# Performance work log

Measured on AMD Instinct MI355X. Metric: run time of the kernel, lower is better.

Reference implementation:

```python
import jax, jax.numpy as jnp
import numpy as np

EPS = 1e-8  # matches torch cosine_similarity default eps


def setup_inputs() -> dict:
    key = jax.random.key(0)
    k1, k2 = jax.random.split(key)
    B, S, D = 64, 512, 768
    logits = jax.random.normal(k1, (B, S, D), dtype=jnp.float32)
    labels = jax.random.randint(k2, (B, S), 0, 10, dtype=jnp.int64)
    return {"logits": logits, "labels": labels, "entity_id": 5}


def reference(logits, labels, entity_id):
    # --- get_proto: mean of token vectors whose label == entity_id,
    # excluding sequence position 0 (label_idx.remove(0) in the original) ---
    B, S, D = logits.shape
    pos = jnp.arange(S)
    ent_mask = (labels == entity_id) & (pos[None, :] != 0)      # [B,S]
    m = ent_mask.astype(logits.dtype)
    num_ent = jnp.maximum(m.sum(), 1.0)
    proto = jnp.einsum('bs,bsd->d', m, logits) / num_ent        # [D]

    # --- CLLoss: mean cosine similarity between proto and every token
    # with a nonzero label ---
    nz_mask = (labels != 0).astype(logits.dtype)                # [B,S]
    dots = jnp.einsum('bsd,d->bs', logits, proto)               # [B,S]
    denom = jnp.linalg.norm(logits, axis=-1) * jnp.linalg.norm(proto)
    sims = dots / jnp.maximum(denom, EPS)                       # [B,S]
    num_tok = jnp.maximum(nz_mask.sum(), 1.0)
    loss = (sims * nz_mask).sum() / num_tok
    return loss
```

## Files before the change

kernel.cpp:

```cpp
#include <hip/hip_runtime.h>
#include <math.h>

#define DD 768
#define S_LEN 512
#define NF4 3
#define NACC (2 * DD + 1)
#define PW 1544
#define GMAIN 1024
#define NYB 16
#define BCHUNK (GMAIN / NYB)

__global__ __launch_bounds__(256) void main_pass(const float* __restrict__ logits,
                                                 const int* __restrict__ labels,
                                                 const int* __restrict__ eid_p,
                                                 int ntok,
                                                 float* __restrict__ partial) {
    const int eid  = *eid_p;
    const int lane = threadIdx.x & 63;
    const int wid  = threadIdx.x >> 6;
    const int gw   = blockIdx.x * 4 + wid;
    const int nw   = GMAIN * 4;

    float u_acc[12], p_acc[12];
#pragma unroll
    for (int j = 0; j < 12; ++j) { u_acc[j] = 0.f; p_acc[j] = 0.f; }
    float tokcnt = 0.f;

    for (int t = gw; t < ntok; t += 2 * nw) {
        const int t2 = t + nw;
        const bool has2 = (t2 < ntok);

        const float4* src0 = (const float4*)(logits + (size_t)t * DD);
        const float4* src1 = (const float4*)(logits + (size_t)(has2 ? t2 : t) * DD);
        float4 f0[NF4], f1[NF4];
#pragma unroll
        for (int k = 0; k < NF4; ++k) f0[k] = src0[k * 64 + lane];
#pragma unroll
        for (int k = 0; k < NF4; ++k) f1[k] = src1[k * 64 + lane];

        float ss0 = 0.f, ss1 = 0.f;
#pragma unroll
        for (int k = 0; k < NF4; ++k) {
            ss0 += f0[k].x * f0[k].x + f0[k].y * f0[k].y + f0[k].z * f0[k].z + f0[k].w * f0[k].w;
            ss1 += f1[k].x * f1[k].x + f1[k].y * f1[k].y + f1[k].z * f1[k].z + f1[k].w * f1[k].w;
        }
#pragma unroll
        for (int o = 32; o > 0; o >>= 1) {
            ss0 += __shfl_xor(ss0, o, 64);
            ss1 += __shfl_xor(ss1, o, 64);
        }

        const int lbl0 = labels[t];
        const int lbl1 = has2 ? labels[t2] : 0;

        const float inv0 = (ss0 > 0.f) ? rsqrtf(ss0) : 0.f;
        const float inv1 = (ss1 > 0.f) ? rsqrtf(ss1) : 0.f;
        const float wu0  = (lbl0 != 0) ? inv0 : 0.f;
        const float wu1  = (has2 && lbl1 != 0) ? inv1 : 0.f;
        const float wp0  = (lbl0 == eid && (t & (S_LEN - 1)) != 0) ? 1.f : 0.f;
        const float wp1  = (has2 && lbl1 == eid && (t2 & (S_LEN - 1)) != 0) ? 1.f : 0.f;
        tokcnt += ((lbl0 != 0) ? 1.f : 0.f) + ((has2 && lbl1 != 0) ? 1.f : 0.f);

#pragma unroll
        for (int k = 0; k < NF4; ++k) {
            u_acc[4 * k + 0] += f0[k].x * wu0 + f1[k].x * wu1;
            u_acc[4 * k + 1] += f0[k].y * wu0 + f1[k].y * wu1;
            u_acc[4 * k + 2] += f0[k].z * wu0 + f1[k].z * wu1;
            u_acc[4 * k + 3] += f0[k].w * wu0 + f1[k].w * wu1;
            p_acc[4 * k + 0] += f0[k].x * wp0 + f1[k].x * wp1;
            p_acc[4 * k + 1] += f0[k].y * wp0 + f1[k].y * wp1;
            p_acc[4 * k + 2] += f0[k].z * wp0 + f1[k].z * wp1;
            p_acc[4 * k + 3] += f0[k].w * wp0 + f1[k].w * wp1;
        }
    }

    __shared__ float sh[NACC];
    for (int i = threadIdx.x; i < NACC; i += 256) sh[i] = 0.f;
    __syncthreads();
    for (int w = 0; w < 4; ++w) {
        if (wid == w) {
#pragma unroll
            for (int k = 0; k < NF4; ++k) {
                const int d = k * 256 + lane * 4;
                sh[d + 0]      += u_acc[4 * k + 0];
                sh[d + 1]      += u_acc[4 * k + 1];
                sh[d + 2]      += u_acc[4 * k + 2];
                sh[d + 3]      += u_acc[4 * k + 3];
                sh[DD + d + 0] += p_acc[4 * k + 0];
                sh[DD + d + 1] += p_acc[4 * k + 1];
                sh[DD + d + 2] += p_acc[4 * k + 2];
                sh[DD + d + 3] += p_acc[4 * k + 3];
            }
            if (lane == 0) sh[2 * DD] += tokcnt;
        }
        __syncthreads();
    }

    float* row = partial + (size_t)blockIdx.x * PW;
    for (int i = threadIdx.x; i < NACC; i += 256) row[i] = sh[i];
}

__global__ __launch_bounds__(256) void reduce_partials(const float* __restrict__ partial,
                                                       float* __restrict__ acc2) {
    const int i = blockIdx.x * 256 + threadIdx.x;
    if (i >= NACC) return;
    const int b0 = blockIdx.y * BCHUNK;
    float s0 = 0.f, s1 = 0.f, s2 = 0.f, s3 = 0.f;
#pragma unroll 4
    for (int j = 0; j < BCHUNK; j += 4) {
        s0 += partial[(size_t)(b0 + j + 0) * PW + i];
        s1 += partial[(size_t)(b0 + j + 1) * PW + i];
        s2 += partial[(size_t)(b0 + j + 2) * PW + i];
        s3 += partial[(size_t)(b0 + j + 3) * PW + i];
    }
    acc2[(size_t)blockIdx.y * PW + i] = (s0 + s1) + (s2 + s3);
}

__global__ __launch_bounds__(256) void finalize(const float* __restrict__ acc2,
                                                float* __restrict__ out) {
    const int tid = threadIdx.x;
    double dup = 0.0, dpp = 0.0;
    for (int i = tid; i < DD; i += 256) {
        float u = 0.f, p = 0.f;
#pragma unroll
        for (int y = 0; y < NYB; ++y) {
            u += acc2[(size_t)y * PW + i];
            p += acc2[(size_t)y * PW + DD + i];
        }
        dup += (double)u * (double)p;
        dpp += (double)p * (double)p;
    }
#pragma unroll
    for (int o = 32; o > 0; o >>= 1) {
        dup += __shfl_down(dup, o, 64);
        dpp += __shfl_down(dpp, o, 64);
    }
    __shared__ double s_up[4], s_pp[4];
    const int lane = tid & 63, wid = tid >> 6;
    if (lane == 0) { s_up[wid] = dup; s_pp[wid] = dpp; }
    __syncthreads();
    if (tid == 0) {
        double up = 0.0, pp = 0.0;
        for (int w = 0; w < 4; ++w) { up += s_up[w]; pp += s_pp[w]; }
        float cnt = 0.f;
#pragma unroll
        for (int y = 0; y < NYB; ++y) cnt += acc2[(size_t)y * PW + 2 * DD];
        float res = 0.f;
        if (pp > 0.0) res = (float)(up / (sqrt(pp) * (double)fmaxf(cnt, 1.f)));
        out[0] = res;
    }
}

extern "C" void kernel_launch(void* const* d_in, const int* in_sizes, int n_in,
                              void* d_out, int out_size, void* d_ws, size_t ws_size,
                              hipStream_t stream) {
    const float* logits = (const float*)d_in[0];
    const int*   labels = (const int*)d_in[1];
    const int*   eid    = (const int*)d_in[2];
    const int ntok = in_sizes[1];

    float* partial = (float*)d_ws;
    float* acc2    = (float*)d_ws + (size_t)GMAIN * PW;

    main_pass<<<GMAIN, 256, 0, stream>>>(logits, labels, eid, ntok, partial);
    reduce_partials<<<dim3(7, NYB), 256, 0, stream>>>(partial, acc2);
    finalize<<<1, 256, 0, stream>>>(acc2, (float*)d_out);
}
```

Before: 158.1 us.

## Skip loading logits for zero-label tokens and prefetch labels per wave

Each wave prefetches its 16 token labels up front and broadcasts them with shuffles. It then skips the logits row load entirely for tokens with label 0 when the entity id is nonzero, and branches instead of using multiplicative masks. The grid is halved and the two-token unroll is removed. This aims to cut memory traffic, but it lowers the number of loads in flight per wave.

```diff
diff --git a/kernel.cpp b/kernel.cpp
--- a/kernel.cpp
+++ b/kernel.cpp
@@ -6,7 +6,8 @@
 #define NF4 3
 #define NACC (2 * DD + 1)
 #define PW 1544
-#define GMAIN 1024
+#define GMAIN 512
+#define NWAVES (GMAIN * 4)
 #define NYB 16
 #define BCHUNK (GMAIN / NYB)
 
@@ -19,58 +20,56 @@
     const int lane = threadIdx.x & 63;
     const int wid  = threadIdx.x >> 6;
     const int gw   = blockIdx.x * 4 + wid;
-    const int nw   = GMAIN * 4;
+
+    int lblv = 0;
+    if (lane < 16) {
+        const int tj = gw + lane * NWAVES;
+        if (tj < ntok) lblv = labels[tj];
+    }
 
     float u_acc[12], p_acc[12];
 #pragma unroll
     for (int j = 0; j < 12; ++j) { u_acc[j] = 0.f; p_acc[j] = 0.f; }
     float tokcnt = 0.f;
 
-    for (int t = gw; t < ntok; t += 2 * nw) {
-        const int t2 = t + nw;
-        const bool has2 = (t2 < ntok);
+    for (int j = 0;; ++j) {
+        const int t = gw + j * NWAVES;
+        if (t >= ntok) break;
+        const int lbl = (j < 16) ? __shfl(lblv, j, 64) : labels[t];
 
-        const float4* src0 = (const float4*)(logits + (size_t)t * DD);
-        const float4* src1 = (const float4*)(logits + (size_t)(has2 ? t2 : t) * DD);
-        float4 f0[NF4], f1[NF4];
+        if (lbl == 0 && eid != 0) continue;
+
+        const float4* src = (const float4*)(logits + (size_t)t * DD);
+        float4 f[NF4];
 #pragma unroll
-        for (int k = 0; k < NF4; ++k) f0[k] = src0[k * 64 + lane];
+        for (int k = 0; k < NF4; ++k) f[k] = src[k * 64 + lane];
+
+        float ss = 0.f;
 #pragma unroll
-        for (int k = 0; k < NF4; ++k) f1[k] = src1[k * 64 + lane];
+        for (int k = 0; k < NF4; ++k)
+            ss += f[k].x * f[k].x + f[k].y * f[k].y + f[k].z * f[k].z + f[k].w * f[k].w;
+#pragma unroll
+        for (int o = 32; o > 0; o >>= 1) ss += __shfl_xor(ss, o, 64);
 
-        float ss0 = 0.f, ss1 = 0.f;
+        if (lbl != 0) {
+            const float inv = (ss > 0.f) ? rsqrtf(ss) : 0.f;
+            tokcnt += 1.f;
 #pragma unroll
-        for (int k = 0; k < NF4; ++k) {
-            ss0 += f0[k].x * f0[k].x + f0[k].y * f0[k].y + f0[k].z * f0[k].z + f0[k].w * f0[k].w;
-            ss1 += f1[k].x * f1[k].x + f1[k].y * f1[k].y + f1[k].z * f1[k].z + f1[k].w * f1[k].w;
+            for (int k = 0; k < NF4; ++k) {
+                u_acc[4 * k + 0] += f[k].x * inv;
+                u_acc[4 * k + 1] += f[k].y * inv;
+                u_acc[4 * k + 2] += f[k].z * inv;
+                u_acc[4 * k + 3] += f[k].w * inv;
+            }
         }
+        if (lbl == eid && (t & (S_LEN - 1)) != 0) {
 #pragma unroll
-        for (int o = 32; o > 0; o >>= 1) {
-            ss0 += __shfl_xor(ss0, o, 64);
-            ss1 += __shfl_xor(ss1, o, 64);
-        }
-
-        const int lbl0 = labels[t];
-        const int lbl1 = has2 ? labels[t2] : 0;
-
-        const float inv0 = (ss0 > 0.f) ? rsqrtf(ss0) : 0.f;
-        const float inv1 = (ss1 > 0.f) ? rsqrtf(ss1) : 0.f;
-        const float wu0  = (lbl0 != 0) ? inv0 : 0.f;
-        const float wu1  = (has2 && lbl1 != 0) ? inv1 : 0.f;
-        const float wp0  = (lbl0 == eid && (t & (S_LEN - 1)) != 0) ? 1.f : 0.f;
-        const float wp1  = (has2 && lbl1 == eid && (t2 & (S_LEN - 1)) != 0) ? 1.f : 0.f;
-        tokcnt += ((lbl0 != 0) ? 1.f : 0.f) + ((has2 && lbl1 != 0) ? 1.f : 0.f);
-
-#pragma unroll
-        for (int k = 0; k < NF4; ++k) {
-            u_acc[4 * k + 0] += f0[k].x * wu0 + f1[k].x * wu1;
-            u_acc[4 * k + 1] += f0[k].y * wu0 + f1[k].y * wu1;
-            u_acc[4 * k + 2] += f0[k].z * wu0 + f1[k].z * wu1;
-            u_acc[4 * k + 3] += f0[k].w * wu0 + f1[k].w * wu1;
-            p_acc[4 * k + 0] += f0[k].x * wp0 + f1[k].x * wp1;
-            p_acc[4 * k + 1] += f0[k].y * wp0 + f1[k].y * wp1;
-            p_acc[4 * k + 2] += f0[k].z * wp0 + f1[k].z * wp1;
-            p_acc[4 * k + 3] += f0[k].w * wp0 + f1[k].w * wp1;
+            for (int k = 0; k < NF4; ++k) {
+                p_acc[4 * k + 0] += f[k].x;
+                p_acc[4 * k + 1] += f[k].y;
+                p_acc[4 * k + 2] += f[k].z;
+                p_acc[4 * k + 3] += f[k].w;
+            }
         }
     }
 
```

Result: no change. 155.2 us (-1.8%).
